# Kernel optimization log

Hardware: AMD Instinct MI355X
Metric: run time of the kernel (lower is better)

## Reference

```python
import jax, jax.numpy as jnp
import numpy as np

V, E, H, W, L = 30000, 300, 512, 20, 512
EPS = 1e-8


def _lstm_dir(x, Wih, Whh):
    # x: [L, E]; PyTorch gate order i, f, g, o; bias=False
    Hh = Whh.shape[1]
    def step(carry, xt):
        h, c = carry
        g = Wih @ xt + Whh @ h
        i, f, gg, o = jnp.split(g, 4)
        c = jax.nn.sigmoid(f) * c + jax.nn.sigmoid(i) * jnp.tanh(gg)
        h = jax.nn.sigmoid(o) * jnp.tanh(c)
        return (h, c), h
    init = (jnp.zeros(Hh, x.dtype), jnp.zeros(Hh, x.dtype))
    _, hs = jax.lax.scan(step, init, x)
    return hs  # [L, H]


def _bilstm(x, Wih_f, Whh_f, Wih_b, Whh_b):
    hf = _lstm_dir(x, Wih_f, Whh_f)
    hb = _lstm_dir(x[::-1], Wih_b, Whh_b)[::-1]
    return jnp.concatenate([hf, hb], axis=-1)  # [L, 2H]


def _wcos_rows(a, b, w):
    # a,b: [L,H] (b may be broadcast of a single vector); w: [W,H] -> [L,W]
    A = a[:, None, :] * w[None]                       # [L,W,H]
    B = jnp.broadcast_to(b, a.shape)[:, None, :] * w[None]
    num = jnp.sum(A * B, axis=-1)
    na = jnp.maximum(jnp.linalg.norm(A, axis=-1), EPS)
    nb = jnp.maximum(jnp.linalg.norm(B, axis=-1), EPS)
    return num / (na * nb)


def _wcos_pair_max(a, b, w):
    # fused pairwise weighted cosine + max over q2: never builds [L1,L2,W,H]
    A = a[:, None, :] * w[None]                       # [L1,W,H]
    B = b[:, None, :] * w[None]                       # [L2,W,H]
    num = jnp.einsum('ikh,jkh->ijk', A, B)            # [L1,L2,W]
    na = jnp.maximum(jnp.linalg.norm(A, axis=-1), EPS)  # [L1,W]
    nb = jnp.maximum(jnp.linalg.norm(B, axis=-1), EPS)  # [L2,W]
    return jnp.max(num / (na[:, None, :] * nb[None, :, :]), axis=1)  # [L1,W]


def _cos_pair(a, b):
    num = a @ b.T                                     # [L1,L2]
    na = jnp.maximum(jnp.linalg.norm(a, axis=-1), EPS)
    nb = jnp.maximum(jnp.linalg.norm(b, axis=-1), EPS)
    return num / (na[:, None] * nb[None, :])


def _model(emb, q1_Wih_f, q1_Whh_f, q1_Wih_b, q1_Whh_b,
           q2_Wih_f, q2_Whh_f, q2_Wih_b, q2_Whh_b,
           W1, W2, W3, W4, W5, W6, q1_ids, q2_ids, l1, l2):
    Hh = W1.shape[1]
    x1 = emb[q1_ids[0, :l1]]                          # [L1,E]
    x2 = emb[q2_ids[0, :l2]]
    q1_outs = _bilstm(x1, q1_Wih_f, q1_Whh_f, q1_Wih_b, q1_Whh_b)
    q2_outs = _bilstm(x2, q2_Wih_f, q2_Whh_f, q2_Wih_b, q2_Whh_b)
    q1p, q1n = q1_outs[:, :Hh], q1_outs[:, Hh:]
    q2p, q2n = q2_outs[:, :Hh], q2_outs[:, Hh:]
    # full matching (vs q2 tail fwd / head bwd)
    m_pos_full = _wcos_rows(q1p, q2p[-1], W1)
    m_neg_full = _wcos_rows(q1n, q2n[0], W2)
    # max-pool matching over all q2 positions
    m_pos_max = _wcos_pair_max(q1p, q2p, W3)
    m_neg_max = _wcos_pair_max(q1n, q2n, W4)
    # attentive matching (cosine attention, mean-by-alpha)
    alpha_pos = _cos_pair(q1p, q2p)                   # [L1,L2]
    q2_pos_att = (alpha_pos @ q2p) / jnp.sum(alpha_pos, axis=1, keepdims=True)
    m_pos_atten = _wcos_rows(q1p, q2_pos_att, W5)
    alpha_neg = _cos_pair(q1n, q2n)
    q2_neg_att = (alpha_neg @ q2n) / jnp.sum(alpha_neg, axis=1, keepdims=True)
    m_neg_atten = _wcos_rows(q1n, q2_neg_att, W5)     # source uses W_5 here (not W_6), kept faithful
    return jnp.stack([m_pos_full, m_neg_full, m_pos_max,
                      m_neg_max, m_pos_atten, m_neg_atten])  # [6,L1,W]


def setup_inputs() -> dict:
    key = jax.random.key(0)
    ks = jax.random.split(key, 20)
    def n(k, shape, s=1.0):
        return jax.random.normal(k, shape, jnp.float32) * s
    return {
        'q1_inputs': jax.random.randint(ks[0], (1, L), 0, V),
        'q2_inputs': jax.random.randint(ks[1], (1, L), 0, V),
        'q1_lens': L,
        'q2_lens': L,
        'emb': n(ks[2], (V, E), 0.1),
        'q1_Wih_f': n(ks[3], (4 * H, E), 0.05), 'q1_Whh_f': n(ks[4], (4 * H, H), 0.05),
        'q1_Wih_b': n(ks[5], (4 * H, E), 0.05), 'q1_Whh_b': n(ks[6], (4 * H, H), 0.05),
        'q2_Wih_f': n(ks[7], (4 * H, E), 0.05), 'q2_Whh_f': n(ks[8], (4 * H, H), 0.05),
        'q2_Wih_b': n(ks[9], (4 * H, E), 0.05), 'q2_Whh_b': n(ks[10], (4 * H, H), 0.05),
        'W1': n(ks[11], (W, H)), 'W2': n(ks[12], (W, H)), 'W3': n(ks[13], (W, H)),
        'W4': n(ks[14], (W, H)), 'W5': n(ks[15], (W, H)), 'W6': n(ks[16], (W, H)),
    }


def reference(q1_inputs, q2_inputs, q1_lens, q2_lens, emb,
              q1_Wih_f, q1_Whh_f, q1_Wih_b, q1_Whh_b,
              q2_Wih_f, q2_Whh_f, q2_Wih_b, q2_Whh_b,
              W1, W2, W3, W4, W5, W6):
    return _model(emb, q1_Wih_f, q1_Whh_f, q1_Wih_b, q1_Whh_b,
                  q2_Wih_f, q2_Whh_f, q2_Wih_b, q2_Whh_b,
                  W1, W2, W3, W4, W5, W6,
                  q1_inputs, q2_inputs, q1_lens, q2_lens)
```

## Files before the change

kernel.cpp:

```cpp
#include <hip/hip_runtime.h>
#include <hip/hip_bf16.h>
#include <math.h>

#define LQ 512
#define HH 512
#define EE 300
#define WW 20
#define G4 2048
#define EPSF 1e-8f
#define RB 32
#define JPB 16

typedef __hip_bfloat16 bf16;
typedef unsigned long long u64;
typedef unsigned int u32;

__device__ __forceinline__ float fast_sigmoid(float x){
  x = fminf(fmaxf(x, -30.f), 30.f);
  return 1.f/(1.f + __expf(-x));
}
__device__ __forceinline__ float fast_tanh(float x){
  x = fminf(fmaxf(x, -15.f), 15.f);
  float e = __expf(2.f*x);
  return (e - 1.f)/(e + 1.f);
}

#define OFF_GIN   0
#define OFF_ALPHA 0
#define OFF_ATT   524288
#define OFF_NRM   1048576
#define OFF_NP    1089536
#define OFF_HS    (4*LQ*G4)
#define OFF_HPUB  (OFF_HS + 4*LQ*HH)
#define WS_NEEDED ((OFF_HPUB + 2*4*LQ*HH) * 4ULL)

__global__ __launch_bounds__(256) void k_sentinel(float* __restrict__ outp, float code)
{
  const int i = blockIdx.x*256 + threadIdx.x;
  if (i < 3072) outp[i] = code;
}

__global__ __launch_bounds__(256) void k_gather_gemm(
    const float* __restrict__ emb, const int* __restrict__ q1_ids, const int* __restrict__ q2_ids,
    const float* __restrict__ wih0, const float* __restrict__ wih1,
    const float* __restrict__ wih2, const float* __restrict__ wih3,
    float* __restrict__ gin)
{
  const int g = blockIdx.z;
  const int* ids = (g < 2) ? q1_ids : q2_ids;
  const float* wih = (g==0)?wih0:(g==1)?wih1:(g==2)?wih2:wih3;
  __shared__ __align__(16) float As[16][68];
  __shared__ __align__(16) float Bs[16][68];
  __shared__ int rowid[64];
  const int tid = threadIdx.x;
  const int tx = tid & 15, ty = tid >> 4;
  const int m0 = blockIdx.y*64, n0 = blockIdx.x*64;
  if (tid < 64) rowid[tid] = ids[m0 + tid];
  __syncthreads();
  float acc[4][4] = {};
  for (int k0 = 0; k0 < EE; k0 += 16) {
    for (int idx = tid; idx < 1024; idx += 256) {
      int r = idx >> 4, kk = idx & 15;
      int k = k0 + kk;
      As[kk][r] = (k < EE) ? emb[(size_t)rowid[r]*EE + k] : 0.f;
      Bs[kk][r] = (k < EE) ? wih[(size_t)(n0+r)*EE + k] : 0.f;
    }
    __syncthreads();
    #pragma unroll
    for (int kk=0;kk<16;kk++){
      float4 a = *reinterpret_cast<const float4*>(&As[kk][ty*4]);
      float4 b = *reinterpret_cast<const float4*>(&Bs[kk][tx*4]);
      acc[0][0]=fmaf(a.x,b.x,acc[0][0]); acc[0][1]=fmaf(a.x,b.y,acc[0][1]);
      acc[0][2]=fmaf(a.x,b.z,acc[0][2]); acc[0][3]=fmaf(a.x,b.w,acc[0][3]);
      acc[1][0]=fmaf(a.y,b.x,acc[1][0]); acc[1][1]=fmaf(a.y,b.y,acc[1][1]);
      acc[1][2]=fmaf(a.y,b.z,acc[1][2]); acc[1][3]=fmaf(a.y,b.w,acc[1][3]);
      acc[2][0]=fmaf(a.z,b.x,acc[2][0]); acc[2][1]=fmaf(a.z,b.y,acc[2][1]);
      acc[2][2]=fmaf(a.z,b.z,acc[2][2]); acc[2][3]=fmaf(a.z,b.w,acc[2][3]);
      acc[3][0]=fmaf(a.w,b.x,acc[3][0]); acc[3][1]=fmaf(a.w,b.y,acc[3][1]);
      acc[3][2]=fmaf(a.w,b.z,acc[3][2]); acc[3][3]=fmaf(a.w,b.w,acc[3][3]);
    }
    __syncthreads();
  }
  float* outp = gin + (size_t)g*LQ*G4;
  #pragma unroll
  for (int u=0;u<4;u++)
    #pragma unroll
    for (int v=0;v<4;v++)
      outp[(size_t)(m0+ty*4+u)*G4 + n0+tx*4+v] = acc[u][v];
}

__global__ __launch_bounds__(512)
__attribute__((amdgpu_waves_per_eu(1,2)))
void k_lstm(
    const float* __restrict__ whh0, const float* __restrict__ whh1,
    const float* __restrict__ whh2, const float* __restrict__ whh3,
    const float* __restrict__ gin, float* __restrict__ hs, u64* __restrict__ hpub)
{
  const int g = (blockIdx.x >> 1) & 3;
  const int b = ((blockIdx.x >> 3) << 1) | (blockIdx.x & 1);
  const float* whh = (g==0)?whh0:(g==1)?whh1:(g==2)?whh2:whh3;
  const int tid = threadIdx.x;
  const int row_local = tid >> 3;
  const int chunk = tid & 7;
  const int gate = row_local >> 4;
  const int jj = row_local & 15;
  const int grow = gate*HH + b*JPB + jj;
  const int rot = chunk;

  const float4* wv4 = reinterpret_cast<const float4*>(whh + (size_t)grow*HH + chunk*64);
  float4 w0  = wv4[(0  + rot) & 15];
  float4 w1  = wv4[(1  + rot) & 15];
  float4 w2  = wv4[(2  + rot) & 15];
  float4 w3  = wv4[(3  + rot) & 15];
  float4 w4  = wv4[(4  + rot) & 15];
  float4 w5  = wv4[(5  + rot) & 15];
  float4 w6  = wv4[(6  + rot) & 15];
  float4 w7  = wv4[(7  + rot) & 15];
  float4 w8  = wv4[(8  + rot) & 15];
  float4 w9  = wv4[(9  + rot) & 15];
  float4 w10 = wv4[(10 + rot) & 15];
  float4 w11 = wv4[(11 + rot) & 15];
  float4 w12 = wv4[(12 + rot) & 15];
  float4 w13 = wv4[(13 + rot) & 15];
  float4 w14 = wv4[(14 + rot) & 15];
  float4 w15 = wv4[(15 + rot) & 15];

  __shared__ __align__(16) float h_lds[HH];
  __shared__ float gdot[64];

  const float* ginp = gin + (size_t)g*LQ*G4;
  float* hsg = hs + (size_t)g*LQ*HH;
  u64* hpg = hpub + (size_t)g*LQ*HH;
  const bool fwd = ((g & 1) == 0);

  float pg_cur = 0.f, pg_nxt = 0.f, creg = 0.f;
  if (tid < 64) {
    const int sidx0 = fwd ? 0 : (LQ-1);
    pg_cur = ginp[(size_t)sidx0*G4 + (size_t)(tid>>4)*HH + b*JPB + (tid&15)];
  }

  for (int s=0; s<LQ; ++s) {
    const int sidx = fwd ? s : (LQ-1-s);
    if (s == 0) {
      h_lds[tid] = 0.f;
      __syncthreads();
    } else {
      const int hidx = fwd ? (s-1) : (LQ-s);
      const u64 want = (u64)(u32)(hidx + 1);
      const u64* hp = hpg + (size_t)hidx*HH + tid;
      u64 v = __hip_atomic_load(hp, __ATOMIC_RELAXED, __HIP_MEMORY_SCOPE_AGENT);
      while ((v >> 32) != want) {
        v = __hip_atomic_load(hp, __ATOMIC_RELAXED, __HIP_MEMORY_SCOPE_AGENT);
      }
      h_lds[tid] = __uint_as_float((u32)v);
      __syncthreads();
    }
    float p0=0.f, p1=0.f, p2=0.f, p3=0.f;
    {
      const float4* hld4 = reinterpret_cast<const float4*>(h_lds) + (chunk << 4);
      #define MSTEP(q, pp) { float4 hh = hld4[((q)+rot)&15]; \
        pp = fmaf(w##q.x, hh.x, pp); pp = fmaf(w##q.y, hh.y, pp); \
        pp = fmaf(w##q.z, hh.z, pp); pp = fmaf(w##q.w, hh.w, pp); }
      MSTEP(0,p0)  MSTEP(1,p1)  MSTEP(2,p2)  MSTEP(3,p3)
      MSTEP(4,p0)  MSTEP(5,p1)  MSTEP(6,p2)  MSTEP(7,p3)
      MSTEP(8,p0)  MSTEP(9,p1)  MSTEP(10,p2) MSTEP(11,p3)
      MSTEP(12,p0) MSTEP(13,p1) MSTEP(14,p2) MSTEP(15,p3)
      #undef MSTEP
    }
    if (tid < 64) {
      const int snx = (s+1 < LQ) ? (s+1) : s;
      const int sidxn = fwd ? snx : (LQ-1-snx);
      pg_nxt = ginp[(size_t)sidxn*G4 + (size_t)(tid>>4)*HH + b*JPB + (tid&15)];
    }
    float partial = (p0 + p1) + (p2 + p3);
    partial += __shfl_xor(partial, 1);
    partial += __shfl_xor(partial, 2);
    partial += __shfl_xor(partial, 4);
    if (chunk == 0) gdot[row_local] = partial;
    __syncthreads();
    if (tid < 64) {
      float x = gdot[tid] + pg_cur;
      const int gt = tid >> 4;
      float t = (gt == 2) ? 2.f*x : x;
      t = fminf(fmaxf(t, -30.f), 30.f);
      float sg = 1.f/(1.f + __expf(-t));
      float y = (gt == 2) ? 2.f*sg - 1.f : sg;
      float vf = __shfl_down(y, 16);
      float vg = __shfl_down(y, 32);
      float vo = __shfl_down(y, 48);
      if (tid < 16) {
        float c = vf*creg + y*vg;
        creg = c;
        float tc = fminf(fmaxf(2.f*c, -30.f), 30.f);
        float th = 2.f/(1.f + __expf(-tc)) - 1.f;
        float h = vo*th;
        const int j = b*JPB + tid;
        u64 pack = ((u64)(u32)(sidx + 1) << 32) | (u64)__float_as_uint(h);
        __hip_atomic_store(hpg + (size_t)sidx*HH + j, pack,
                           __ATOMIC_RELAXED, __HIP_MEMORY_SCOPE_AGENT);
        hsg[(size_t)sidx*HH + j] = h;
      }
      pg_cur = pg_nxt;
    }
  }
}

__global__ __launch_bounds__(256) void k_norms(
    const float* __restrict__ hs, const float* __restrict__ W3, const float* __restrict__ W4,
    float* __restrict__ nrm, float* __restrict__ np_)
{
  const int l = blockIdx.x;
  const int which = blockIdx.y;
  const int hsidx = (which==0)?0:(which==1)?2:(which==2)?1:3;
  const float* P = hs + (size_t)hsidx*LQ*HH + (size_t)l*HH;
  const float* Wt = (which < 2) ? W3 : W4;
  const int tid = threadIdx.x;
  const int w = tid >> 6, ln = tid & 63;
  __shared__ float p[HH];
  p[tid] = P[tid]; p[tid+256] = P[tid+256];
  __syncthreads();
  if (w == 0) {
    float v = 0.f;
    #pragma unroll
    for (int q=0;q<8;q++){ float x = p[ln+64*q]; v = fmaf(x,x,v); }
    #pragma unroll
    for (int o=32;o>0;o>>=1) v += __shfl_xor(v,o);
    if (ln==0) np_[which*LQ + l] = fmaxf(sqrtf(v), EPSF);
  }
  for (int k=w; k<WW; k+=4){
    const float* wk = Wt + (size_t)k*HH;
    float v = 0.f;
    #pragma unroll
    for (int q=0;q<8;q++){
      int e = ln + 64*q;
      float a = p[e]*wk[e];
      v = fmaf(a,a,v);
    }
    #pragma unroll
    for (int o=32;o>0;o>>=1) v += __shfl_xor(v,o);
    if (ln==0) nrm[(size_t)which*LQ*WW + (size_t)l*WW + k] = fmaxf(sqrtf(v), EPSF);
  }
}

__global__ __launch_bounds__(256) void k_alpha(
    const float* __restrict__ hs, const float* __restrict__ np_, float* __restrict__ alpha)
{
  const int z = blockIdx.z;
  const float* A = hs + (size_t)(z?1:0)*LQ*HH;
  const float* B = hs + (size_t)(z?3:2)*LQ*HH;
  const float* nai = np_ + (z?2:0)*LQ;
  const float* nbj = np_ + (z?3:1)*LQ;
  float* outp = alpha + (size_t)z*LQ*LQ;
  __shared__ __align__(16) float As[16][68], Bs[16][68];
  const int tid = threadIdx.x;
  const int tx = tid & 15, ty = tid >> 4;
  const int i0 = blockIdx.y*64, j0 = blockIdx.x*64;
  float acc[4][4] = {};
  for (int k0=0;k0<HH;k0+=16){
    for (int idx=tid; idx<1024; idx+=256){
      int r = idx>>4, kk = idx&15;
      As[kk][r] = A[(size_t)(i0+r)*HH + k0+kk];
      Bs[kk][r] = B[(size_t)(j0+r)*HH + k0+kk];
    }
    __syncthreads();
    #pragma unroll
    for (int kk=0;kk<16;kk++){
      float4 a = *reinterpret_cast<const float4*>(&As[kk][ty*4]);
      float4 b = *reinterpret_cast<const float4*>(&Bs[kk][tx*4]);
      acc[0][0]=fmaf(a.x,b.x,acc[0][0]); acc[0][1]=fmaf(a.x,b.y,acc[0][1]);
      acc[0][2]=fmaf(a.x,b.z,acc[0][2]); acc[0][3]=fmaf(a.x,b.w,acc[0][3]);
      acc[1][0]=fmaf(a.y,b.x,acc[1][0]); acc[1][1]=fmaf(a.y,b.y,acc[1][1]);
      acc[1][2]=fmaf(a.y,b.z,acc[1][2]); acc[1][3]=fmaf(a.y,b.w,acc[1][3]);
      acc[2][0]=fmaf(a.z,b.x,acc[2][0]); acc[2][1]=fmaf(a.z,b.y,acc[2][1]);
      acc[2][2]=fmaf(a.z,b.z,acc[2][2]); acc[2][3]=fmaf(a.z,b.w,acc[2][3]);
      acc[3][0]=fmaf(a.w,b.x,acc[3][0]); acc[3][1]=fmaf(a.w,b.y,acc[3][1]);
      acc[3][2]=fmaf(a.w,b.z,acc[3][2]); acc[3][3]=fmaf(a.w,b.w,acc[3][3]);
    }
    __syncthreads();
  }
  #pragma unroll
  for (int u=0;u<4;u++){
    float ina = 1.f/nai[i0+ty*4+u];
    #pragma unroll
    for (int v=0;v<4;v++)
      outp[(size_t)(i0+ty*4+u)*LQ + j0+tx*4+v] = acc[u][v]*ina/nbj[j0+tx*4+v];
  }
}

__global__ __launch_bounds__(256) void k_att(
    const float* __restrict__ alpha, const float* __restrict__ hs,
    float* __restrict__ att)
{
  const int z = blockIdx.z;
  const float* A = alpha + (size_t)z*LQ*LQ;
  const float* B = hs + (size_t)(z?3:2)*LQ*HH;
  float* outp = att + (size_t)z*LQ*HH;
  __shared__ __align__(16) float As[16][68], Bs[16][68];
  const int tid = threadIdx.x;
  const int tx = tid & 15, ty = tid >> 4;
  const int i0 = blockIdx.y*64, h0 = blockIdx.x*64;
  float acc[4][4] = {};
  float rsum[4] = {};
  for (int j0=0;j0<LQ;j0+=16){
    for (int idx=tid; idx<1024; idx+=256){
      int r = idx>>4, kk = idx&15;
      As[kk][r] = A[(size_t)(i0+r)*LQ + j0+kk];
    }
    for (int idx=tid; idx<1024; idx+=256){
      int jjr = idx>>6, hh = idx&63;
      Bs[jjr][hh] = B[(size_t)(j0+jjr)*HH + h0+hh];
    }
    __syncthreads();
    #pragma unroll
    for (int kk=0;kk<16;kk++){
      float4 a = *reinterpret_cast<const float4*>(&As[kk][ty*4]);
      float4 b = *reinterpret_cast<const float4*>(&Bs[kk][tx*4]);
      rsum[0]+=a.x; rsum[1]+=a.y; rsum[2]+=a.z; rsum[3]+=a.w;
      acc[0][0]=fmaf(a.x,b.x,acc[0][0]); acc[0][1]=fmaf(a.x,b.y,acc[0][1]);
      acc[0][2]=fmaf(a.x,b.z,acc[0][2]); acc[0][3]=fmaf(a.x,b.w,acc[0][3]);
      acc[1][0]=fmaf(a.y,b.x,acc[1][0]); acc[1][1]=fmaf(a.y,b.y,acc[1][1]);
      acc[1][2]=fmaf(a.y,b.z,acc[1][2]); acc[1][3]=fmaf(a.y,b.w,acc[1][3]);
      acc[2][0]=fmaf(a.z,b.x,acc[2][0]); acc[2][1]=fmaf(a.z,b.y,acc[2][1]);
      acc[2][2]=fmaf(a.z,b.z,acc[2][2]); acc[2][3]=fmaf(a.z,b.w,acc[2][3]);
      acc[3][0]=fmaf(a.w,b.x,acc[3][0]); acc[3][1]=fmaf(a.w,b.y,acc[3][1]);
      acc[3][2]=fmaf(a.w,b.z,acc[3][2]); acc[3][3]=fmaf(a.w,b.w,acc[3][3]);
    }
    __syncthreads();
  }
  #pragma unroll
  for (int u=0;u<4;u++){
    float inv = 1.f/rsum[u];
    #pragma unroll
    for (int v=0;v<4;v++)
      outp[(size_t)(i0+ty*4+u)*HH + h0+tx*4+v] = acc[u][v]*inv;
  }
}

__global__ __launch_bounds__(256) void k_wcos(
    const float* __restrict__ hs, const float* __restrict__ att,
    const float* __restrict__ W1, const float* __restrict__ W2, const float* __restrict__ W5,
    float* __restrict__ outp)
{
  const int l = blockIdx.x;
  const int which = blockIdx.y;
  const int tid = threadIdx.x;
  const float* a; const float* c; const float* Wt; int m;
  switch (which) {
    case 0:  a = hs + (size_t)0*LQ*HH + (size_t)l*HH; c = hs + (size_t)2*LQ*HH + (size_t)(LQ-1)*HH; Wt = W1; m = 0; break;
    case 1:  a = hs + (size_t)1*LQ*HH + (size_t)l*HH; c = hs + (size_t)3*LQ*HH;                     Wt = W2; m = 1; break;
    case 2:  a = hs + (size_t)0*LQ*HH + (size_t)l*HH; c = att + (size_t)0*LQ*HH + (size_t)l*HH;     Wt = W5; m = 4; break;
    default: a = hs + (size_t)1*LQ*HH + (size_t)l*HH; c = att + (size_t)1*LQ*HH + (size_t)l*HH;     Wt = W5; m = 5; break;
  }
  __shared__ float av[HH], cv[HH];
  const int w = tid >> 6, ln = tid & 63;
  av[tid]=a[tid]; av[tid+256]=a[tid+256];
  cv[tid]=c[tid]; cv[tid+256]=c[tid+256];
  __syncthreads();
  for (int k=w; k<WW; k+=4){
    const float* wk = Wt + (size_t)k*HH;
    float num=0.f, na=0.f, nc=0.f;
    #pragma unroll
    for (int q=0;q<8;q++){
      int e = ln + 64*q;
      float w1 = wk[e];
      float aw = av[e]*w1;
      float cw = cv[e]*w1;
      num = fmaf(aw,cw,num);
      na  = fmaf(aw,aw,na);
      nc  = fmaf(cw,cw,nc);
    }
    #pragma unroll
    for (int o=32;o>0;o>>=1){
      num += __shfl_xor(num,o);
      na  += __shfl_xor(na,o);
      nc  += __shfl_xor(nc,o);
    }
    if (ln==0){
      float d = fmaxf(sqrtf(na),EPSF)*fmaxf(sqrtf(nc),EPSF);
      outp[((size_t)m*LQ + l)*WW + k] = num/d;
    }
  }
}

__global__ __launch_bounds__(256) void k_pairmax(
    const float* __restrict__ hs, const float* __restrict__ W3, const float* __restrict__ W4,
    const float* __restrict__ nrm, float* __restrict__ outp)
{
  const int k  = blockIdx.x;
  const int it = blockIdx.y;
  const int mm = blockIdx.z;
  const float* A = hs + (size_t)(mm?1:0)*LQ*HH;
  const float* B = hs + (size_t)(mm?3:2)*LQ*HH;
  const float* Wt = mm ? W4 : W3;
  const float* na = nrm + (size_t)(mm?2:0)*LQ*WW;
  const float* nb = nrm + (size_t)(mm?3:1)*LQ*WW;
  const int tid = threadIdx.x;
  const int tx = tid & 15, ty = tid >> 4;
  __shared__ float w2[HH];
  __shared__ float nbinv[LQ];
  __shared__ __align__(16) float As[16][68], Bs[16][68];
  for (int h=tid; h<HH; h+=256){ float wv = Wt[(size_t)k*HH + h]; w2[h]=wv*wv; }
  for (int j=tid; j<LQ; j+=256){ nbinv[j] = 1.f/nb[(size_t)j*WW + k]; }
  __syncthreads();
  const int i0 = it*64;
  float vmax[4] = {-3.4e38f,-3.4e38f,-3.4e38f,-3.4e38f};
  for (int j0=0;j0<LQ;j0+=64){
    float acc[4][4] = {};
    for (int k0=0;k0<HH;k0+=16){
      for (int idx=tid; idx<1024; idx+=256){
        int r=idx>>4, kk=idx&15;
        As[kk][r] = A[(size_t)(i0+r)*HH + k0+kk] * w2[k0+kk];
      }
      for (int idx=tid; idx<1024; idx+=256){
        int r=idx>>4, kk=idx&15;
        Bs[kk][r] = B[(size_t)(j0+r)*HH + k0+kk];
      }
      __syncthreads();
      #pragma unroll
      for (int kk=0;kk<16;kk++){
        float4 a = *reinterpret_cast<const float4*>(&As[kk][ty*4]);
        float4 b = *reinterpret_cast<const float4*>(&Bs[kk][tx*4]);
        acc[0][0]=fmaf(a.x,b.x,acc[0][0]); acc[0][1]=fmaf(a.x,b.y,acc[0][1]);
        acc[0][2]=fmaf(a.x,b.z,acc[0][2]); acc[0][3]=fmaf(a.x,b.w,acc[0][3]);
        acc[1][0]=fmaf(a.y,b.x,acc[1][0]); acc[1][1]=fmaf(a.y,b.y,acc[1][1]);
        acc[1][2]=fmaf(a.y,b.z,acc[1][2]); acc[1][3]=fmaf(a.y,b.w,acc[1][3]);
        acc[2][0]=fmaf(a.z,b.x,acc[2][0]); acc[2][1]=fmaf(a.z,b.y,acc[2][1]);
        acc[2][2]=fmaf(a.z,b.z,acc[2][2]); acc[2][3]=fmaf(a.z,b.w,acc[2][3]);
        acc[3][0]=fmaf(a.w,b.x,acc[3][0]); acc[3][1]=fmaf(a.w,b.y,acc[3][1]);
        acc[3][2]=fmaf(a.w,b.z,acc[3][2]); acc[3][3]=fmaf(a.w,b.w,acc[3][3]);
      }
      __syncthreads();
    }
    #pragma unroll
    for (int v=0;v<4;v++){
      float nv = nbinv[j0+tx*4+v];
      #pragma unroll
      for (int u=0;u<4;u++)
        vmax[u] = fmaxf(vmax[u], acc[u][v]*nv);
    }
  }
  #pragma unroll
  for (int o=1;o<16;o<<=1){
    #pragma unroll
    for (int u=0;u<4;u++)
      vmax[u] = fmaxf(vmax[u], __shfl_xor(vmax[u], o, 16));
  }
  if (tx==0){
    #pragma unroll
    for (int u=0;u<4;u++){
      int i = i0 + ty*4 + u;
      outp[((size_t)(mm+2)*LQ + i)*WW + k] = vmax[u] / na[(size_t)i*WW + k];
    }
  }
}

extern "C" void kernel_launch(void* const* d_in, const int* in_sizes, int n_in,
                              void* d_out, int out_size, void* d_ws, size_t ws_size,
                              hipStream_t stream)
{
  float* outp = (float*)d_out;

  float code = 0.f;
  if (n_in != 19)                    code = 101.f;
  else if (in_sizes[0]  != 512)      code = 102.f;
  else if (in_sizes[4]  != 9000000)  code = 104.f;
  else if (in_sizes[6]  != 1048576)  code = 106.f;
  else if (out_size     != 61440)    code = 108.f;
  else if (ws_size      < WS_NEEDED) code = 109.f;
  if (code != 0.f) {
    k_sentinel<<<12, 256, 0, stream>>>(outp, code);
    return;
  }

  const int* q1_ids = (const int*)d_in[0];
  const int* q2_ids = (const int*)d_in[1];
  const float* emb      = (const float*)d_in[4];
  const float* q1_wih_f = (const float*)d_in[5];
  const float* q1_whh_f = (const float*)d_in[6];
  const float* q1_wih_b = (const float*)d_in[7];
  const float* q1_whh_b = (const float*)d_in[8];
  const float* q2_wih_f = (const float*)d_in[9];
  const float* q2_whh_f = (const float*)d_in[10];
  const float* q2_wih_b = (const float*)d_in[11];
  const float* q2_whh_b = (const float*)d_in[12];
  const float* W1 = (const float*)d_in[13];
  const float* W2 = (const float*)d_in[14];
  const float* W3 = (const float*)d_in[15];
  const float* W4 = (const float*)d_in[16];
  const float* W5 = (const float*)d_in[17];
  float* ws = (float*)d_ws;

  float* gin   = ws + OFF_GIN;
  float* hsv   = ws + OFF_HS;
  u64*   hpub  = (u64*)(ws + OFF_HPUB);
  float* alpha = ws + OFF_ALPHA;
  float* att   = ws + OFF_ATT;
  float* nrm   = ws + OFF_NRM;
  float* np_   = ws + OFF_NP;

  k_gather_gemm<<<dim3(32,8,4), 256, 0, stream>>>(emb, q1_ids, q2_ids,
      q1_wih_f, q1_wih_b, q2_wih_f, q2_wih_b, gin);
  k_lstm<<<dim3(4*RB), 512, 0, stream>>>(q1_whh_f, q1_whh_b, q2_whh_f, q2_whh_b,
      gin, hsv, hpub);
  k_norms<<<dim3(LQ,4), 256, 0, stream>>>(hsv, W3, W4, nrm, np_);
  k_alpha<<<dim3(8,8,2), 256, 0, stream>>>(hsv, np_, alpha);
  k_att<<<dim3(8,8,2), 256, 0, stream>>>(alpha, hsv, att);
  k_wcos<<<dim3(LQ,4), 256, 0, stream>>>(hsv, att, W1, W2, W5, outp);
  k_pairmax<<<dim3(WW,8,2), 256, 0, stream>>>(hsv, W3, W4, nrm, outp);
}
```

Baseline: 1.502 ms.

## Restructure pairwise max kernel to share A/B tiles across all weight rows

The pairwise weighted-cosine max kernel previously ran one block per weight row k and recomputed the A·B inner products for each of the 20 rows. It now tiles over (i,j) blocks, forms the elementwise a*b product once per h, and contracts it against 10 squared weight rows at a time. This reuses the loaded A/B tiles across weight rows and raises the grid from 320 to 512 blocks. The cost is a larger register footprint (80 accumulators per thread), partial maxima written to workspace, and an extra reduction kernel launch.

```diff
diff --git a/kernel.cpp b/kernel.cpp
--- a/kernel.cpp
+++ b/kernel.cpp
@@ -30,6 +30,7 @@
 #define OFF_ATT   524288
 #define OFF_NRM   1048576
 #define OFF_NP    1089536
+#define OFF_PMP   1179648
 #define OFF_HS    (4*LQ*G4)
 #define OFF_HPUB  (OFF_HS + 4*LQ*HH)
 #define WS_NEEDED ((OFF_HPUB + 2*4*LQ*HH) * 4ULL)
@@ -384,74 +385,110 @@
 
 __global__ __launch_bounds__(256) void k_pairmax(
     const float* __restrict__ hs, const float* __restrict__ W3, const float* __restrict__ W4,
-    const float* __restrict__ nrm, float* __restrict__ outp)
-{
-  const int k  = blockIdx.x;
-  const int it = blockIdx.y;
-  const int mm = blockIdx.z;
+    const float* __restrict__ nrm, float* __restrict__ pm_part)
+{
+  const int it = blockIdx.x;
+  const int jt = blockIdx.y;
+  const int z  = blockIdx.z;
+  const int mm = z >> 1, kh = z & 1;
+  const int k0 = kh*10;
   const float* A = hs + (size_t)(mm?1:0)*LQ*HH;
   const float* B = hs + (size_t)(mm?3:2)*LQ*HH;
   const float* Wt = mm ? W4 : W3;
+  const float* nb = nrm + (size_t)(mm?3:1)*LQ*WW;
+  const int tid = threadIdx.x;
+  const int tx = tid & 31;
+  const int ty = tid >> 5;
+  const int i0 = it*64;
+  const int j  = jt*32 + tx;
+
+  __shared__ __align__(16) float As[64][128];
+  __shared__ __align__(16) float Bs[32][132];
+  __shared__ __align__(16) float Ws[10][128];
+
+  float acc[8][10];
+  #pragma unroll
+  for (int r=0;r<8;r++)
+    #pragma unroll
+    for (int q=0;q<10;q++) acc[r][q]=0.f;
+
+  for (int hc=0; hc<4; ++hc){
+    const int hbase = hc*128;
+    for (int idx=tid; idx<2048; idx+=256){
+      int row = idx >> 5, c4 = idx & 31;
+      *reinterpret_cast<float4*>(&As[row][c4*4]) =
+        *reinterpret_cast<const float4*>(&A[(size_t)(i0+row)*HH + hbase + c4*4]);
+    }
+    for (int idx=tid; idx<1024; idx+=256){
+      int row = idx >> 5, c4 = idx & 31;
+      *reinterpret_cast<float4*>(&Bs[row][c4*4]) =
+        *reinterpret_cast<const float4*>(&B[(size_t)(jt*32+row)*HH + hbase + c4*4]);
+    }
+    for (int idx=tid; idx<1280; idx+=256){
+      int kk = idx >> 7, cc = idx & 127;
+      float wv = Wt[(size_t)(k0+kk)*HH + hbase + cc];
+      Ws[kk][cc] = wv*wv;
+    }
+    __syncthreads();
+    #pragma unroll 2
+    for (int h4=0; h4<32; ++h4){
+      float4 b = *reinterpret_cast<const float4*>(&Bs[tx][h4*4]);
+      float4 sa[8];
+      #pragma unroll
+      for (int r=0;r<8;r++){
+        float4 a = *reinterpret_cast<const float4*>(&As[ty*8+r][h4*4]);
+        sa[r].x = a.x*b.x; sa[r].y = a.y*b.y;
+        sa[r].z = a.z*b.z; sa[r].w = a.w*b.w;
+      }
+      #pragma unroll
+      for (int q=0;q<10;q++){
+        float4 w = *reinterpret_cast<const float4*>(&Ws[q][h4*4]);
+        #pragma unroll
+        for (int r=0;r<8;r++){
+          acc[r][q] = fmaf(sa[r].x, w.x, acc[r][q]);
+          acc[r][q] = fmaf(sa[r].y, w.y, acc[r][q]);
+          acc[r][q] = fmaf(sa[r].z, w.z, acc[r][q]);
+          acc[r][q] = fmaf(sa[r].w, w.w, acc[r][q]);
+        }
+      }
+    }
+    __syncthreads();
+  }
+
+  float nbv[10];
+  #pragma unroll
+  for (int q=0;q<10;q++) nbv[q] = 1.f / nb[(size_t)j*WW + k0 + q];
+  #pragma unroll
+  for (int r=0;r<8;r++){
+    #pragma unroll
+    for (int q=0;q<10;q++){
+      float v = acc[r][q] * nbv[q];
+      #pragma unroll
+      for (int o=1;o<32;o<<=1) v = fmaxf(v, __shfl_xor(v, o, 32));
+      if (tx==0)
+        pm_part[((((size_t)z*8 + it)*16 + jt)*64 + (ty*8+r))*10 + q] = v;
+    }
+  }
+}
+
+__global__ __launch_bounds__(256) void k_pmfin(
+    const float* __restrict__ pm_part, const float* __restrict__ nrm,
+    float* __restrict__ outp)
+{
+  const int idx = blockIdx.x*256 + threadIdx.x;
+  if (idx >= 2*LQ*WW) return;
+  const int mm = idx / (LQ*WW);
+  const int rem = idx - mm*LQ*WW;
+  const int i = rem / WW, k = rem % WW;
+  const int it = i >> 6, il = i & 63;
+  const int kh = k / 10, kl = k % 10;
+  const int z = mm*2 + kh;
+  float v = -3.4e38f;
+  #pragma unroll
+  for (int jt=0; jt<16; ++jt)
+    v = fmaxf(v, pm_part[((((size_t)z*8 + it)*16 + jt)*64 + il)*10 + kl]);
   const float* na = nrm + (size_t)(mm?2:0)*LQ*WW;
-  const float* nb = nrm + (size_t)(mm?3:1)*LQ*WW;
-  const int tid = threadIdx.x;
-  const int tx = tid & 15, ty = tid >> 4;
-  __shared__ float w2[HH];
-  __shared__ float nbinv[LQ];
-  __shared__ __align__(16) float As[16][68], Bs[16][68];
-  for (int h=tid; h<HH; h+=256){ float wv = Wt[(size_t)k*HH + h]; w2[h]=wv*wv; }
-  for (int j=tid; j<LQ; j+=256){ nbinv[j] = 1.f/nb[(size_t)j*WW + k]; }
-  __syncthreads();
-  const int i0 = it*64;
-  float vmax[4] = {-3.4e38f,-3.4e38f,-3.4e38f,-3.4e38f};
-  for (int j0=0;j0<LQ;j0+=64){
-    float acc[4][4] = {};
-    for (int k0=0;k0<HH;k0+=16){
-      for (int idx=tid; idx<1024; idx+=256){
-        int r=idx>>4, kk=idx&15;
-        As[kk][r] = A[(size_t)(i0+r)*HH + k0+kk] * w2[k0+kk];
-      }
-      for (int idx=tid; idx<1024; idx+=256){
-        int r=idx>>4, kk=idx&15;
-        Bs[kk][r] = B[(size_t)(j0+r)*HH + k0+kk];
-      }
-      __syncthreads();
-      #pragma unroll
-      for (int kk=0;kk<16;kk++){
-        float4 a = *reinterpret_cast<const float4*>(&As[kk][ty*4]);
-        float4 b = *reinterpret_cast<const float4*>(&Bs[kk][tx*4]);
-        acc[0][0]=fmaf(a.x,b.x,acc[0][0]); acc[0][1]=fmaf(a.x,b.y,acc[0][1]);
-        acc[0][2]=fmaf(a.x,b.z,acc[0][2]); acc[0][3]=fmaf(a.x,b.w,acc[0][3]);
-        acc[1][0]=fmaf(a.y,b.x,acc[1][0]); acc[1][1]=fmaf(a.y,b.y,acc[1][1]);
-        acc[1][2]=fmaf(a.y,b.z,acc[1][2]); acc[1][3]=fmaf(a.y,b.w,acc[1][3]);
-        acc[2][0]=fmaf(a.z,b.x,acc[2][0]); acc[2][1]=fmaf(a.z,b.y,acc[2][1]);
-        acc[2][2]=fmaf(a.z,b.z,acc[2][2]); acc[2][3]=fmaf(a.z,b.w,acc[2][3]);
-        acc[3][0]=fmaf(a.w,b.x,acc[3][0]); acc[3][1]=fmaf(a.w,b.y,acc[3][1]);
-        acc[3][2]=fmaf(a.w,b.z,acc[3][2]); acc[3][3]=fmaf(a.w,b.w,acc[3][3]);
-      }
-      __syncthreads();
-    }
-    #pragma unroll
-    for (int v=0;v<4;v++){
-      float nv = nbinv[j0+tx*4+v];
-      #pragma unroll
-      for (int u=0;u<4;u++)
-        vmax[u] = fmaxf(vmax[u], acc[u][v]*nv);
-    }
-  }
-  #pragma unroll
-  for (int o=1;o<16;o<<=1){
-    #pragma unroll
-    for (int u=0;u<4;u++)
-      vmax[u] = fmaxf(vmax[u], __shfl_xor(vmax[u], o, 16));
-  }
-  if (tx==0){
-    #pragma unroll
-    for (int u=0;u<4;u++){
-      int i = i0 + ty*4 + u;
-      outp[((size_t)(mm+2)*LQ + i)*WW + k] = vmax[u] / na[(size_t)i*WW + k];
-    }
-  }
+  outp[((size_t)(mm+2)*LQ + i)*WW + k] = v / na[(size_t)i*WW + k];
 }
 
 extern "C" void kernel_launch(void* const* d_in, const int* in_sizes, int n_in,
@@ -497,6 +534,7 @@
   float* att   = ws + OFF_ATT;
   float* nrm   = ws + OFF_NRM;
   float* np_   = ws + OFF_NP;
+  float* pmp   = ws + OFF_PMP;
 
   k_gather_gemm<<<dim3(32,8,4), 256, 0, stream>>>(emb, q1_ids, q2_ids,
       q1_wih_f, q1_wih_b, q2_wih_f, q2_wih_b, gin);
@@ -506,5 +544,6 @@
   k_alpha<<<dim3(8,8,2), 256, 0, stream>>>(hsv, np_, alpha);
   k_att<<<dim3(8,8,2), 256, 0, stream>>>(alpha, hsv, att);
   k_wcos<<<dim3(LQ,4), 256, 0, stream>>>(hsv, att, W1, W2, W5, outp);
-  k_pairmax<<<dim3(WW,8,2), 256, 0, stream>>>(hsv, W3, W4, nrm, outp);
-}
+  k_pairmax<<<dim3(8,16,4), 256, 0, stream>>>(hsv, W3, W4, nrm, pmp);
+  k_pmfin<<<dim3(80), 256, 0, stream>>>(pmp, nrm, outp);
+}
```

Result: faster. 1.225 ms (-18.4%).
